# Kernel tuning notes

Measured on AMD Instinct MI355X. Metric: run time of the kernel, lower is better.

The kernel has to match this reference:

```python
import jax, jax.numpy as jnp
import numpy as np

CLIP_MIN = 0.0  # recurrent_clip_min resolved in build() when -1
CLIP_MAX = 1.0  # recurrent_clip_max default when timesteps unknown


def setup_inputs() -> dict:
    key = jax.random.key(0)
    k1, k2, k3 = jax.random.split(key, 3)
    B, T, D, U = 64, 512, 256, 512
    x = jax.random.normal(k1, (B, T, D), dtype=jnp.float32)
    h0 = jnp.zeros((B, U), dtype=jnp.float32)
    W = jax.random.normal(k2, (D, U), dtype=jnp.float32) * (1.0 / np.sqrt(D))
    u = jax.random.uniform(k3, (U,), dtype=jnp.float32)  # uniform in clip range
    b = jnp.zeros((U,), dtype=jnp.float32)
    return {"x": x, "h0": h0, "W": W, "u": u, "b": b}


def reference(x, h0, W, u, b):
    # IndRNN: h_t = relu(x_t @ W + h_{t-1} * u + b), u clipped to [0, 1]
    u_c = jnp.clip(u, CLIP_MIN, CLIP_MAX)
    # One-time input projection for all timesteps: [B,T,U]
    proj = jnp.einsum("btd,du->btu", x, W) + b
    proj_t = jnp.swapaxes(proj, 0, 1)  # [T,B,U] for scan over time

    def step(h, p_t):
        h_new = jax.nn.relu(p_t + h * u_c)
        return h_new, h_new

    _, hs = jax.lax.scan(step, h0, proj_t)  # hs: [T,B,U]
    return jnp.swapaxes(hs, 0, 1)  # [B,T,U]
```

## Files before the change

### kernel.cpp

```cpp
#include <hip/hip_runtime.h>


__device__ __forceinline__ unsigned short f2bf(float f) {
    unsigned int u = __float_as_uint(f);
    unsigned int r = (u + 0x7FFF + ((u >> 16) & 1)) >> 16;
    return (unsigned short)r;
}

typedef __bf16 bf16x8 __attribute__((ext_vector_type(8)));
typedef float f32x4 __attribute__((ext_vector_type(4)));

typedef const unsigned char __attribute__((address_space(1))) gc_t;
typedef unsigned char __attribute__((address_space(3))) lds_t;

__device__ __forceinline__ void gl_lds16(const void* g, void* l) {
    __builtin_amdgcn_global_load_lds((gc_t*)g, (lds_t*)l, 16, 0, 0);
}

__global__ __launch_bounds__(256) void conv_x(
    const float* __restrict__ x, unsigned short* __restrict__ xb, int n4)
{
    int i = blockIdx.x * blockDim.x + threadIdx.x;
    if (i >= n4) return;
    float4 v = *(const float4*)(x + (long)i * 4);
    ushort4 o;
    o.x = f2bf(v.x); o.y = f2bf(v.y); o.z = f2bf(v.z); o.w = f2bf(v.w);
    *(ushort4*)(xb + (long)i * 4) = o;
}

__global__ __launch_bounds__(256) void conv_wt(
    const float* __restrict__ W, unsigned short* __restrict__ Wt, int K, int N)
{
    int idx = blockIdx.x * blockDim.x + threadIdx.x;
    int kq = K >> 2;
    if (idx >= N * kq) return;
    int n = idx / kq;
    int k4 = (idx - n * kq) * 4;
    ushort4 o;
    o.x = f2bf(W[(long)(k4 + 0) * N + n]);
    o.y = f2bf(W[(long)(k4 + 1) * N + n]);
    o.z = f2bf(W[(long)(k4 + 2) * N + n]);
    o.w = f2bf(W[(long)(k4 + 3) * N + n]);
    *(ushort4*)(Wt + (long)n * K + k4) = o;
}

#define TC 64
#define GN 128

__global__ __launch_bounds__(256, 1) void indrnn_fused(
    const unsigned short* __restrict__ xb,
    const unsigned short* __restrict__ wt,
    const float* __restrict__ bias,
    const float* __restrict__ h0,
    const float* __restrict__ uvec,
    float* __restrict__ out,
    int B, int T, int U)
{
    __shared__ char Xs[TC * 512];
    __shared__ char Ps[GN * TC * 4];

    const int tid  = threadIdx.x;
    const int lane = tid & 63;
    const int w    = tid >> 6;
    const int m    = lane & 15;
    const int quad = lane >> 4;
    const int b    = blockIdx.x;
    const int n0   = blockIdx.y * GN;
    const int tq   = (w >> 1) * 32;
    const int cq   = (w & 1) * 64;

    bf16x8 bfr[4][8];
#pragma unroll
    for (int j = 0; j < 4; ++j)
#pragma unroll
        for (int kt = 0; kt < 8; ++kt)
            bfr[j][kt] = *(const bf16x8*)(
                wt + (long)(n0 + cq + j * 16 + m) * 256 + kt * 32 + quad * 8);

    float bb[4];
#pragma unroll
    for (int j = 0; j < 4; ++j) bb[j] = bias[n0 + cq + j * 16 + m];

    float uc = 0.0f, h = 0.0f;
    if (tid < GN) {
        uc = fminf(fmaxf(uvec[n0 + tid], 0.0f), 1.0f);
        h  = h0[(long)b * U + n0 + tid];
    }

    const unsigned short* xrow = xb + (long)b * T * 256;
    const int p  = lane & 31;
    const int hh = lane >> 5;

#pragma unroll
    for (int i = 0; i < 8; ++i) {
        int blk = i * 4 + w;
        int row = blk * 2 + hh;
        int gp  = p ^ (row & 15);
        gl_lds16(xrow + (long)row * 256 + gp * 8, &Xs[blk * 1024]);
    }
    asm volatile("s_waitcnt vmcnt(0)" ::: "memory");
    __builtin_amdgcn_sched_barrier(0);
    __syncthreads();

    const int nch = T / TC;
    for (int c = 0; c < nch; ++c) {
        f32x4 acc[2][4];
#pragma unroll
        for (int i = 0; i < 2; ++i)
#pragma unroll
            for (int j = 0; j < 4; ++j) acc[i][j] = (f32x4){0.f, 0.f, 0.f, 0.f};

#pragma unroll
        for (int kt = 0; kt < 8; ++kt) {
            const int off = (((kt * 4 + quad) ^ m) * 16);
            bf16x8 a0 = *(const bf16x8*)(Xs + (tq + m) * 512 + off);
            bf16x8 a1 = *(const bf16x8*)(Xs + (tq + 16 + m) * 512 + off);
#pragma unroll
            for (int j = 0; j < 4; ++j) {
                acc[0][j] = __builtin_amdgcn_mfma_f32_16x16x32_bf16(
                    a0, bfr[j][kt], acc[0][j], 0, 0, 0);
                acc[1][j] = __builtin_amdgcn_mfma_f32_16x16x32_bf16(
                    a1, bfr[j][kt], acc[1][j], 0, 0, 0);
            }
        }

#pragma unroll
        for (int i = 0; i < 2; ++i)
#pragma unroll
            for (int j = 0; j < 4; ++j) {
                f32x4 v = acc[i][j];
                f32x4 vb = {v[0] + bb[j], v[1] + bb[j], v[2] + bb[j], v[3] + bb[j]};
                int col = cq + j * 16 + m;
                int g   = (tq >> 2) + i * 4 + quad;
                *(f32x4*)(Ps + col * 256 + (((g ^ (col & 7)) << 4))) = vb;
            }
        __syncthreads();

        if (c + 1 < nch) {
            const unsigned short* gb = xrow + (long)(c + 1) * TC * 256;
#pragma unroll
            for (int i = 0; i < 8; ++i) {
                int blk = i * 4 + w;
                int row = blk * 2 + hh;
                int gp  = p ^ (row & 15);
                gl_lds16(gb + (long)row * 256 + gp * 8, &Xs[blk * 1024]);
            }
        }

        if (tid < GN) {
            f32x4 pv[16];
            const int ub = tid * 256;
            const int ux = (tid & 7) << 4;
#pragma unroll
            for (int gg = 0; gg < 16; ++gg)
                pv[gg] = *(const f32x4*)(Ps + ub + ((gg << 4) ^ ux));
            float* og = out + ((long)b * T + c * TC) * U + n0 + tid;
#pragma unroll
            for (int gg = 0; gg < 16; ++gg)
#pragma unroll
                for (int e = 0; e < 4; ++e) {
                    h = fmaxf(fmaf(h, uc, pv[gg][e]), 0.0f);
                    og[(long)(gg * 4 + e) * U] = h;
                }
        }

        asm volatile("s_waitcnt vmcnt(0)" ::: "memory");
        __builtin_amdgcn_sched_barrier(0);
        __syncthreads();
    }
}

#define BM 128
#define BN 128
#define BK 8

__global__ __launch_bounds__(256) void indrnn_gemm_bias(
    const float* __restrict__ A, const float* __restrict__ Bm,
    const float* __restrict__ bias, float* __restrict__ C,
    int M, int N, int K)
{
    __shared__ float As[BK][BM];
    __shared__ float Bs[BK][BN];
    const int tid = threadIdx.x;
    const int row0 = blockIdx.x * BM, col0 = blockIdx.y * BN;
    const int tx = tid & 15, ty = tid >> 4;
    float acc[8][8];
#pragma unroll
    for (int i = 0; i < 8; ++i)
#pragma unroll
        for (int j = 0; j < 8; ++j) acc[i][j] = 0.0f;
    const int am = tid >> 1, ak = (tid & 1) * 4;
    const int bk = tid >> 5, bn = (tid & 31) * 4;
    const float* Aptr = A + (long)(row0 + am) * K + ak;
    const float* Bptr = Bm + (long)bk * N + col0 + bn;
    for (int kt = 0; kt < K; kt += BK) {
        float4 av = *(const float4*)(Aptr + kt);
        float4 bv = *(const float4*)(Bptr + (long)kt * N);
        As[ak + 0][am] = av.x; As[ak + 1][am] = av.y;
        As[ak + 2][am] = av.z; As[ak + 3][am] = av.w;
        *(float4*)&Bs[bk][bn] = bv;
        __syncthreads();
#pragma unroll
        for (int k = 0; k < BK; ++k) {
            float4 a0 = *(const float4*)&As[k][ty * 4];
            float4 a1 = *(const float4*)&As[k][64 + ty * 4];
            float4 b0 = *(const float4*)&Bs[k][tx * 4];
            float4 b1 = *(const float4*)&Bs[k][64 + tx * 4];
            float a[8] = {a0.x, a0.y, a0.z, a0.w, a1.x, a1.y, a1.z, a1.w};
            float bb2[8] = {b0.x, b0.y, b0.z, b0.w, b1.x, b1.y, b1.z, b1.w};
#pragma unroll
            for (int i = 0; i < 8; ++i)
#pragma unroll
                for (int j = 0; j < 8; ++j)
                    acc[i][j] = fmaf(a[i], bb2[j], acc[i][j]);
        }
        __syncthreads();
    }
    float bb[8];
#pragma unroll
    for (int j = 0; j < 4; ++j) {
        bb[j] = bias[col0 + tx * 4 + j];
        bb[j + 4] = bias[col0 + 64 + tx * 4 + j];
    }
#pragma unroll
    for (int i = 0; i < 8; ++i) {
        const int r = (i < 4) ? (ty * 4 + i) : (64 + ty * 4 + (i - 4));
        float* crow = C + (long)(row0 + r) * N + col0;
        float4 v0 = {acc[i][0] + bb[0], acc[i][1] + bb[1], acc[i][2] + bb[2], acc[i][3] + bb[3]};
        float4 v1 = {acc[i][4] + bb[4], acc[i][5] + bb[5], acc[i][6] + bb[6], acc[i][7] + bb[7]};
        *(float4*)(crow + tx * 4) = v0;
        *(float4*)(crow + 64 + tx * 4) = v1;
    }
}

#define SCAN_UNROLL 32

__global__ __launch_bounds__(256) void indrnn_scan(
    float* __restrict__ out, const float* __restrict__ h0,
    const float* __restrict__ u, int B, int T, int U)
{
    const int idx = blockIdx.x * blockDim.x + threadIdx.x;
    if (idx >= B * U) return;
    const int b = idx / U;
    const int un = idx - b * U;
    const float uc = fminf(fmaxf(u[un], 0.0f), 1.0f);
    float h = h0[(long)b * U + un];
    float* p = out + (long)b * T * U + un;
    for (int t = 0; t < T; t += SCAN_UNROLL) {
        float pv[SCAN_UNROLL];
#pragma unroll
        for (int i = 0; i < SCAN_UNROLL; ++i)
            pv[i] = p[(long)(t + i) * U];
#pragma unroll
        for (int i = 0; i < SCAN_UNROLL; ++i) {
            h = fmaxf(fmaf(h, uc, pv[i]), 0.0f);
            pv[i] = h;
        }
#pragma unroll
        for (int i = 0; i < SCAN_UNROLL; ++i)
            p[(long)(t + i) * U] = pv[i];
    }
}

extern "C" void kernel_launch(void* const* d_in, const int* in_sizes, int n_in,
                              void* d_out, int out_size, void* d_ws, size_t ws_size,
                              hipStream_t stream) {
    const float* x  = (const float*)d_in[0];
    const float* h0 = (const float*)d_in[1];
    const float* W  = (const float*)d_in[2];
    const float* u  = (const float*)d_in[3];
    const float* b  = (const float*)d_in[4];
    float* out = (float*)d_out;

    const int U = in_sizes[3];
    const int B = in_sizes[1] / U;
    const int D = in_sizes[2] / U;
    const int T = in_sizes[0] / (B * D);
    const int M = B * T;

    const size_t xb_bytes = (size_t)M * D * sizeof(unsigned short);
    const size_t wt_bytes = (size_t)U * D * sizeof(unsigned short);
    const bool fused_ok = (D == 256) && (U % GN == 0) && (T % TC == 0) &&
                          (ws_size >= xb_bytes + wt_bytes);

    if (fused_ok) {
        unsigned short* xb = (unsigned short*)d_ws;
        unsigned short* wt = (unsigned short*)((char*)d_ws + xb_bytes);

        const int n4 = (M * D) / 4;
        conv_x<<<(n4 + 255) / 256, 256, 0, stream>>>(x, xb, n4);
        const int nwt = U * (D / 4);
        conv_wt<<<(nwt + 255) / 256, 256, 0, stream>>>(W, wt, D, U);

        dim3 g(B, U / GN);
        indrnn_fused<<<g, 256, 0, stream>>>(xb, wt, b, h0, u, out, B, T, U);
    } else {
        dim3 ggrid(M / BM, U / BN);
        indrnn_gemm_bias<<<ggrid, 256, 0, stream>>>(x, W, b, out, M, U, D);
        const int nthreads = B * U;
        indrnn_scan<<<(nthreads + 255) / 256, 256, 0, stream>>>(out, h0, u, B, T, U);
    }
}
```

Baseline: 118.7 us.

## Warp-specialize fused IndRNN into producer GEMM and consumer scan waves

Splits the fused kernel's four waves into two producer waves that do the bf16 MFMA projection and two consumer waves that run the sequential scan and write output. Double-buffered LDS tiles and shared-memory flag spin-waits replace the per-chunk __syncthreads, so the next chunk's GEMM can overlap the current chunk's scan. It also merges the two bf16 conversion kernels into one launch. Producer waves now hold all of the B fragments (bfr[8][8]), which raises register pressure. The volatile LDS polling depends on memory-ordering assumptions that could be fragile.

```diff
diff --git a/kernel.cpp b/kernel.cpp
--- a/kernel.cpp
+++ b/kernel.cpp
@@ -17,31 +17,31 @@
     __builtin_amdgcn_global_load_lds((gc_t*)g, (lds_t*)l, 16, 0, 0);
 }
 
-__global__ __launch_bounds__(256) void conv_x(
-    const float* __restrict__ x, unsigned short* __restrict__ xb, int n4)
+__global__ __launch_bounds__(256) void conv_xw(
+    const float* __restrict__ x, unsigned short* __restrict__ xb, int n4,
+    const float* __restrict__ W, unsigned short* __restrict__ Wt,
+    int K, int N, int xblocks)
 {
-    int i = blockIdx.x * blockDim.x + threadIdx.x;
-    if (i >= n4) return;
-    float4 v = *(const float4*)(x + (long)i * 4);
-    ushort4 o;
-    o.x = f2bf(v.x); o.y = f2bf(v.y); o.z = f2bf(v.z); o.w = f2bf(v.w);
-    *(ushort4*)(xb + (long)i * 4) = o;
-}
-
-__global__ __launch_bounds__(256) void conv_wt(
-    const float* __restrict__ W, unsigned short* __restrict__ Wt, int K, int N)
-{
-    int idx = blockIdx.x * blockDim.x + threadIdx.x;
-    int kq = K >> 2;
-    if (idx >= N * kq) return;
-    int n = idx / kq;
-    int k4 = (idx - n * kq) * 4;
-    ushort4 o;
-    o.x = f2bf(W[(long)(k4 + 0) * N + n]);
-    o.y = f2bf(W[(long)(k4 + 1) * N + n]);
-    o.z = f2bf(W[(long)(k4 + 2) * N + n]);
-    o.w = f2bf(W[(long)(k4 + 3) * N + n]);
-    *(ushort4*)(Wt + (long)n * K + k4) = o;
+    if ((int)blockIdx.x < xblocks) {
+        int i = blockIdx.x * 256 + threadIdx.x;
+        if (i >= n4) return;
+        float4 v = *(const float4*)(x + (long)i * 4);
+        ushort4 o;
+        o.x = f2bf(v.x); o.y = f2bf(v.y); o.z = f2bf(v.z); o.w = f2bf(v.w);
+        *(ushort4*)(xb + (long)i * 4) = o;
+    } else {
+        int idx = (blockIdx.x - xblocks) * 256 + threadIdx.x;
+        int kq = K >> 2;
+        if (idx >= N * kq) return;
+        int n = idx / kq;
+        int k4 = (idx - n * kq) * 4;
+        ushort4 o;
+        o.x = f2bf(W[(long)(k4 + 0) * N + n]);
+        o.y = f2bf(W[(long)(k4 + 1) * N + n]);
+        o.z = f2bf(W[(long)(k4 + 2) * N + n]);
+        o.w = f2bf(W[(long)(k4 + 3) * N + n]);
+        *(ushort4*)(Wt + (long)n * K + k4) = o;
+    }
 }
 
 #define TC 64
@@ -56,8 +56,9 @@
     float* __restrict__ out,
     int B, int T, int U)
 {
-    __shared__ char Xs[TC * 512];
-    __shared__ char Ps[GN * TC * 4];
+    __shared__ char Xs[2][TC * 512];
+    __shared__ char Ps[2][GN * TC * 4];
+    __shared__ int  flg[8];
 
     const int tid  = threadIdx.x;
     const int lane = tid & 63;
@@ -66,94 +67,112 @@
     const int quad = lane >> 4;
     const int b    = blockIdx.x;
     const int n0   = blockIdx.y * GN;
-    const int tq   = (w >> 1) * 32;
-    const int cq   = (w & 1) * 64;
-
-    bf16x8 bfr[4][8];
-#pragma unroll
-    for (int j = 0; j < 4; ++j)
-#pragma unroll
-        for (int kt = 0; kt < 8; ++kt)
-            bfr[j][kt] = *(const bf16x8*)(
-                wt + (long)(n0 + cq + j * 16 + m) * 256 + kt * 32 + quad * 8);
-
-    float bb[4];
-#pragma unroll
-    for (int j = 0; j < 4; ++j) bb[j] = bias[n0 + cq + j * 16 + m];
-
-    float uc = 0.0f, h = 0.0f;
-    if (tid < GN) {
-        uc = fminf(fmaxf(uvec[n0 + tid], 0.0f), 1.0f);
-        h  = h0[(long)b * U + n0 + tid];
-    }
-
-    const unsigned short* xrow = xb + (long)b * T * 256;
-    const int p  = lane & 31;
-    const int hh = lane >> 5;
-
-#pragma unroll
-    for (int i = 0; i < 8; ++i) {
-        int blk = i * 4 + w;
-        int row = blk * 2 + hh;
-        int gp  = p ^ (row & 15);
-        gl_lds16(xrow + (long)row * 256 + gp * 8, &Xs[blk * 1024]);
-    }
-    asm volatile("s_waitcnt vmcnt(0)" ::: "memory");
-    __builtin_amdgcn_sched_barrier(0);
+
+    if (tid < 8) flg[tid] = 0;
     __syncthreads();
 
+    volatile int* vf = (volatile int*)flg;
     const int nch = T / TC;
-    for (int c = 0; c < nch; ++c) {
-        f32x4 acc[2][4];
-#pragma unroll
-        for (int i = 0; i < 2; ++i)
-#pragma unroll
-            for (int j = 0; j < 4; ++j) acc[i][j] = (f32x4){0.f, 0.f, 0.f, 0.f};
-
-#pragma unroll
-        for (int kt = 0; kt < 8; ++kt) {
-            const int off = (((kt * 4 + quad) ^ m) * 16);
-            bf16x8 a0 = *(const bf16x8*)(Xs + (tq + m) * 512 + off);
-            bf16x8 a1 = *(const bf16x8*)(Xs + (tq + 16 + m) * 512 + off);
-#pragma unroll
-            for (int j = 0; j < 4; ++j) {
-                acc[0][j] = __builtin_amdgcn_mfma_f32_16x16x32_bf16(
-                    a0, bfr[j][kt], acc[0][j], 0, 0, 0);
-                acc[1][j] = __builtin_amdgcn_mfma_f32_16x16x32_bf16(
-                    a1, bfr[j][kt], acc[1][j], 0, 0, 0);
+
+    if (w >= 2) {
+        const int r0 = (w - 2) * 32;
+        const int p  = lane & 31;
+        const int hh = lane >> 5;
+        const unsigned short* xrow = xb + (long)b * T * 256;
+
+        bf16x8 bfr[8][8];
+#pragma unroll
+        for (int j = 0; j < 8; ++j)
+#pragma unroll
+            for (int kt = 0; kt < 8; ++kt)
+                bfr[j][kt] = *(const bf16x8*)(
+                    wt + (long)(n0 + j * 16 + m) * 256 + kt * 32 + quad * 8);
+
+        float bb[8];
+#pragma unroll
+        for (int j = 0; j < 8; ++j) bb[j] = bias[n0 + j * 16 + m];
+
+#pragma unroll
+        for (int l = 0; l < 16; ++l) {
+            int row = r0 + l * 2 + hh;
+            int gp  = p ^ (row & 15);
+            gl_lds16(xrow + (long)row * 256 + gp * 8,
+                     &Xs[0][r0 * 512 + l * 1024]);
+        }
+
+        for (int c = 0; c < nch; ++c) {
+            const int buf = c & 1, nb = buf ^ 1;
+
+            asm volatile("s_waitcnt vmcnt(0)" ::: "memory");
+            __builtin_amdgcn_sched_barrier(0);
+
+            if (c + 1 < nch) {
+                const unsigned short* gb = xrow + (long)(c + 1) * TC * 256;
+#pragma unroll
+                for (int l = 0; l < 16; ++l) {
+                    int row = r0 + l * 2 + hh;
+                    int gp  = p ^ (row & 15);
+                    gl_lds16(gb + (long)row * 256 + gp * 8,
+                             &Xs[nb][r0 * 512 + l * 1024]);
+                }
             }
-        }
-
-#pragma unroll
-        for (int i = 0; i < 2; ++i)
-#pragma unroll
-            for (int j = 0; j < 4; ++j) {
-                f32x4 v = acc[i][j];
-                f32x4 vb = {v[0] + bb[j], v[1] + bb[j], v[2] + bb[j], v[3] + bb[j]};
-                int col = cq + j * 16 + m;
-                int g   = (tq >> 2) + i * 4 + quad;
-                *(f32x4*)(Ps + col * 256 + (((g ^ (col & 7)) << 4))) = vb;
+
+            f32x4 acc[2][8];
+#pragma unroll
+            for (int i = 0; i < 2; ++i)
+#pragma unroll
+                for (int j = 0; j < 8; ++j) acc[i][j] = (f32x4){0.f, 0.f, 0.f, 0.f};
+
+#pragma unroll
+            for (int kt = 0; kt < 8; ++kt) {
+                const int off = (((kt * 4 + quad) ^ m) * 16);
+                bf16x8 a0 = *(const bf16x8*)(&Xs[buf][(r0 + m) * 512 + off]);
+                bf16x8 a1 = *(const bf16x8*)(&Xs[buf][(r0 + 16 + m) * 512 + off]);
+#pragma unroll
+                for (int j = 0; j < 8; ++j) {
+                    acc[0][j] = __builtin_amdgcn_mfma_f32_16x16x32_bf16(
+                        a0, bfr[j][kt], acc[0][j], 0, 0, 0);
+                    acc[1][j] = __builtin_amdgcn_mfma_f32_16x16x32_bf16(
+                        a1, bfr[j][kt], acc[1][j], 0, 0, 0);
+                }
             }
-        __syncthreads();
-
-        if (c + 1 < nch) {
-            const unsigned short* gb = xrow + (long)(c + 1) * TC * 256;
-#pragma unroll
-            for (int i = 0; i < 8; ++i) {
-                int blk = i * 4 + w;
-                int row = blk * 2 + hh;
-                int gp  = p ^ (row & 15);
-                gl_lds16(gb + (long)row * 256 + gp * 8, &Xs[blk * 1024]);
-            }
-        }
-
-        if (tid < GN) {
+
+            while (vf[4 + buf] < c - 1 || vf[6 + buf] < c - 1) {}
+            asm volatile("" ::: "memory");
+            __builtin_amdgcn_sched_barrier(0);
+
+#pragma unroll
+            for (int i = 0; i < 2; ++i)
+#pragma unroll
+                for (int j = 0; j < 8; ++j) {
+                    f32x4 v = acc[i][j];
+                    f32x4 vb = {v[0] + bb[j], v[1] + bb[j],
+                                v[2] + bb[j], v[3] + bb[j]};
+                    int col = j * 16 + m;
+                    int g   = (r0 >> 2) + i * 4 + quad;
+                    *(f32x4*)(&Ps[buf][col * 256 + (((g ^ (col & 7)) << 4))]) = vb;
+                }
+            asm volatile("s_waitcnt lgkmcnt(0)" ::: "memory");
+            if (lane == 0) vf[(w - 2) * 2 + buf] = c + 1;
+        }
+    } else {
+        const float uc = fminf(fmaxf(uvec[n0 + tid], 0.0f), 1.0f);
+        float h = h0[(long)b * U + n0 + tid];
+        const int ub = tid * 256;
+        const int ux = (tid & 7) << 4;
+
+        for (int c = 0; c < nch; ++c) {
+            const int buf = c & 1;
+
+            while (vf[0 + buf] < c + 1 || vf[2 + buf] < c + 1) {}
+            asm volatile("" ::: "memory");
+            __builtin_amdgcn_sched_barrier(0);
+
             f32x4 pv[16];
-            const int ub = tid * 256;
-            const int ux = (tid & 7) << 4;
 #pragma unroll
             for (int gg = 0; gg < 16; ++gg)
-                pv[gg] = *(const f32x4*)(Ps + ub + ((gg << 4) ^ ux));
+                pv[gg] = *(const f32x4*)(&Ps[buf][ub + ((gg << 4) ^ ux)]);
+
             float* og = out + ((long)b * T + c * TC) * U + n0 + tid;
 #pragma unroll
             for (int gg = 0; gg < 16; ++gg)
@@ -162,11 +181,10 @@
                     h = fmaxf(fmaf(h, uc, pv[gg][e]), 0.0f);
                     og[(long)(gg * 4 + e) * U] = h;
                 }
-        }
-
-        asm volatile("s_waitcnt vmcnt(0)" ::: "memory");
-        __builtin_amdgcn_sched_barrier(0);
-        __syncthreads();
+
+            asm volatile("s_waitcnt lgkmcnt(0)" ::: "memory");
+            if (lane == 0) vf[4 + w * 2 + buf] = c + 1;
+        }
     }
 }
 
@@ -288,9 +306,11 @@
         unsigned short* wt = (unsigned short*)((char*)d_ws + xb_bytes);
 
         const int n4 = (M * D) / 4;
-        conv_x<<<(n4 + 255) / 256, 256, 0, stream>>>(x, xb, n4);
         const int nwt = U * (D / 4);
-        conv_wt<<<(nwt + 255) / 256, 256, 0, stream>>>(W, wt, D, U);
+        const int xblocks = (n4 + 255) / 256;
+        const int wblocks = (nwt + 255) / 256;
+        conv_xw<<<xblocks + wblocks, 256, 0, stream>>>(
+            x, xb, n4, W, wt, D, U, xblocks);
 
         dim3 g(B, U / GN);
         indrnn_fused<<<g, 256, 0, stream>>>(xb, wt, b, h0, u, out, B, T, U);
```

Measured after the change: 121.5 us. +2.4%, slower.

## Fuse bf16 conversion of x and W into the fused IndRNN kernel

Applied to the files above, without the earlier changes.

Removes the separate conv_x and conv_wt pre-passes and the workspace round trip. The fused kernel now streams fp32 x rows straight into LDS with a wider swizzled layout and converts to bf16 in registers just before the MFMAs. W is gathered and converted per block at kernel start. The aim is to drop two kernel launches and the extra global write and read of a bf16 copy of x. In exchange, each block reads twice as many bytes of x, LDS use doubles, and every timestep chunk now does conversion work in the inner loop.

```diff
diff --git a/kernel.cpp b/kernel.cpp
--- a/kernel.cpp
+++ b/kernel.cpp
@@ -1,11 +1,5 @@
 #include <hip/hip_runtime.h>
 
-
-__device__ __forceinline__ unsigned short f2bf(float f) {
-    unsigned int u = __float_as_uint(f);
-    unsigned int r = (u + 0x7FFF + ((u >> 16) & 1)) >> 16;
-    return (unsigned short)r;
-}
 
 typedef __bf16 bf16x8 __attribute__((ext_vector_type(8)));
 typedef float f32x4 __attribute__((ext_vector_type(4)));
@@ -17,46 +11,28 @@
     __builtin_amdgcn_global_load_lds((gc_t*)g, (lds_t*)l, 16, 0, 0);
 }
 
-__global__ __launch_bounds__(256) void conv_x(
-    const float* __restrict__ x, unsigned short* __restrict__ xb, int n4)
-{
-    int i = blockIdx.x * blockDim.x + threadIdx.x;
-    if (i >= n4) return;
-    float4 v = *(const float4*)(x + (long)i * 4);
-    ushort4 o;
-    o.x = f2bf(v.x); o.y = f2bf(v.y); o.z = f2bf(v.z); o.w = f2bf(v.w);
-    *(ushort4*)(xb + (long)i * 4) = o;
-}
-
-__global__ __launch_bounds__(256) void conv_wt(
-    const float* __restrict__ W, unsigned short* __restrict__ Wt, int K, int N)
-{
-    int idx = blockIdx.x * blockDim.x + threadIdx.x;
-    int kq = K >> 2;
-    if (idx >= N * kq) return;
-    int n = idx / kq;
-    int k4 = (idx - n * kq) * 4;
-    ushort4 o;
-    o.x = f2bf(W[(long)(k4 + 0) * N + n]);
-    o.y = f2bf(W[(long)(k4 + 1) * N + n]);
-    o.z = f2bf(W[(long)(k4 + 2) * N + n]);
-    o.w = f2bf(W[(long)(k4 + 3) * N + n]);
-    *(ushort4*)(Wt + (long)n * K + k4) = o;
+__device__ __forceinline__ bf16x8 cvt8(f32x4 lo, f32x4 hi) {
+    bf16x8 r;
+    r[0] = (__bf16)lo[0]; r[1] = (__bf16)lo[1];
+    r[2] = (__bf16)lo[2]; r[3] = (__bf16)lo[3];
+    r[4] = (__bf16)hi[0]; r[5] = (__bf16)hi[1];
+    r[6] = (__bf16)hi[2]; r[7] = (__bf16)hi[3];
+    return r;
 }
 
 #define TC 64
 #define GN 128
 
 __global__ __launch_bounds__(256, 1) void indrnn_fused(
-    const unsigned short* __restrict__ xb,
-    const unsigned short* __restrict__ wt,
+    const float* __restrict__ x,
+    const float* __restrict__ W,
     const float* __restrict__ bias,
     const float* __restrict__ h0,
     const float* __restrict__ uvec,
     float* __restrict__ out,
     int B, int T, int U)
 {
-    __shared__ char Xs[TC * 512];
+    __shared__ char Xs[TC * 1024];
     __shared__ char Ps[GN * TC * 4];
 
     const int tid  = threadIdx.x;
@@ -69,13 +45,27 @@
     const int tq   = (w >> 1) * 32;
     const int cq   = (w & 1) * 64;
 
+    const float* xrow = x + (long)b * T * 256;
+
+#pragma unroll
+    for (int i = 0; i < 16; ++i) {
+        int row = i * 4 + w;
+        int sg  = lane ^ (row & 15);
+        gl_lds16(xrow + (long)row * 256 + sg * 4, &Xs[row * 1024]);
+    }
+
     bf16x8 bfr[4][8];
 #pragma unroll
     for (int j = 0; j < 4; ++j)
 #pragma unroll
-        for (int kt = 0; kt < 8; ++kt)
-            bfr[j][kt] = *(const bf16x8*)(
-                wt + (long)(n0 + cq + j * 16 + m) * 256 + kt * 32 + quad * 8);
+        for (int kt = 0; kt < 8; ++kt) {
+            const float* wp = W + (long)(kt * 32 + quad * 8) * U
+                                + (n0 + cq + j * 16 + m);
+            bf16x8 f;
+#pragma unroll
+            for (int e = 0; e < 8; ++e) f[e] = (__bf16)wp[(long)e * U];
+            bfr[j][kt] = f;
+        }
 
     float bb[4];
 #pragma unroll
@@ -87,17 +77,6 @@
         h  = h0[(long)b * U + n0 + tid];
     }
 
-    const unsigned short* xrow = xb + (long)b * T * 256;
-    const int p  = lane & 31;
-    const int hh = lane >> 5;
-
-#pragma unroll
-    for (int i = 0; i < 8; ++i) {
-        int blk = i * 4 + w;
-        int row = blk * 2 + hh;
-        int gp  = p ^ (row & 15);
-        gl_lds16(xrow + (long)row * 256 + gp * 8, &Xs[blk * 1024]);
-    }
     asm volatile("s_waitcnt vmcnt(0)" ::: "memory");
     __builtin_amdgcn_sched_barrier(0);
     __syncthreads();
@@ -112,9 +91,16 @@
 
 #pragma unroll
         for (int kt = 0; kt < 8; ++kt) {
-            const int off = (((kt * 4 + quad) ^ m) * 16);
-            bf16x8 a0 = *(const bf16x8*)(Xs + (tq + m) * 512 + off);
-            bf16x8 a1 = *(const bf16x8*)(Xs + (tq + 16 + m) * 512 + off);
+            const int g0 = ((kt * 8 + quad * 2 + 0) ^ m) << 4;
+            const int g1 = ((kt * 8 + quad * 2 + 1) ^ m) << 4;
+            const char* r0p = Xs + (tq + m) * 1024;
+            const char* r1p = Xs + (tq + 16 + m) * 1024;
+            f32x4 a0lo = *(const f32x4*)(r0p + g0);
+            f32x4 a0hi = *(const f32x4*)(r0p + g1);
+            f32x4 a1lo = *(const f32x4*)(r1p + g0);
+            f32x4 a1hi = *(const f32x4*)(r1p + g1);
+            bf16x8 a0 = cvt8(a0lo, a0hi);
+            bf16x8 a1 = cvt8(a1lo, a1hi);
 #pragma unroll
             for (int j = 0; j < 4; ++j) {
                 acc[0][j] = __builtin_amdgcn_mfma_f32_16x16x32_bf16(
@@ -137,13 +123,12 @@
         __syncthreads();
 
         if (c + 1 < nch) {
-            const unsigned short* gb = xrow + (long)(c + 1) * TC * 256;
-#pragma unroll
-            for (int i = 0; i < 8; ++i) {
-                int blk = i * 4 + w;
-                int row = blk * 2 + hh;
-                int gp  = p ^ (row & 15);
-                gl_lds16(gb + (long)row * 256 + gp * 8, &Xs[blk * 1024]);
+            const float* gb = xrow + (long)(c + 1) * TC * 256;
+#pragma unroll
+            for (int i = 0; i < 16; ++i) {
+                int row = i * 4 + w;
+                int sg  = lane ^ (row & 15);
+                gl_lds16(gb + (long)row * 256 + sg * 4, &Xs[row * 1024]);
             }
         }
 
@@ -278,22 +263,11 @@
     const int T = in_sizes[0] / (B * D);
     const int M = B * T;
 
-    const size_t xb_bytes = (size_t)M * D * sizeof(unsigned short);
-    const size_t wt_bytes = (size_t)U * D * sizeof(unsigned short);
-    const bool fused_ok = (D == 256) && (U % GN == 0) && (T % TC == 0) &&
-                          (ws_size >= xb_bytes + wt_bytes);
+    const bool fused_ok = (D == 256) && (U % GN == 0) && (T % TC == 0);
 
     if (fused_ok) {
-        unsigned short* xb = (unsigned short*)d_ws;
-        unsigned short* wt = (unsigned short*)((char*)d_ws + xb_bytes);
-
-        const int n4 = (M * D) / 4;
-        conv_x<<<(n4 + 255) / 256, 256, 0, stream>>>(x, xb, n4);
-        const int nwt = U * (D / 4);
-        conv_wt<<<(nwt + 255) / 256, 256, 0, stream>>>(W, wt, D, U);
-
         dim3 g(B, U / GN);
-        indrnn_fused<<<g, 256, 0, stream>>>(xb, wt, b, h0, u, out, B, T, U);
+        indrnn_fused<<<g, 256, 0, stream>>>(x, W, b, h0, u, out, B, T, U);
     } else {
         dim3 ggrid(M / BM, U / BN);
         indrnn_gemm_bias<<<ggrid, 256, 0, stream>>>(x, W, b, out, M, U, D);
```

Measured after the change: 116.4 us. No clear change (-1.9%).

## Double-buffer X chunks in LDS and fold W conversion into fused kernel

Applied to the files above, without the earlier changes.

Removes the separate conv_wt launch, so the fused kernel now reads fp32 W directly and converts it to bf16 in registers while the first X chunk is loading. The X staging buffer in LDS becomes double-buffered, and the next chunk's prefetch is issued before the MFMA work so it overlaps both the GEMM and the serial scan. The scan threads now wait with a partial vmcnt so their output stores are not drained every chunk. The risks are a doubled LDS footprint, strided scalar W loads at kernel start, and an fp32-to-bf16 cast whose rounding may differ from f2bf.

```diff
diff --git a/kernel.cpp b/kernel.cpp
--- a/kernel.cpp
+++ b/kernel.cpp
@@ -28,35 +28,19 @@
     *(ushort4*)(xb + (long)i * 4) = o;
 }
 
-__global__ __launch_bounds__(256) void conv_wt(
-    const float* __restrict__ W, unsigned short* __restrict__ Wt, int K, int N)
-{
-    int idx = blockIdx.x * blockDim.x + threadIdx.x;
-    int kq = K >> 2;
-    if (idx >= N * kq) return;
-    int n = idx / kq;
-    int k4 = (idx - n * kq) * 4;
-    ushort4 o;
-    o.x = f2bf(W[(long)(k4 + 0) * N + n]);
-    o.y = f2bf(W[(long)(k4 + 1) * N + n]);
-    o.z = f2bf(W[(long)(k4 + 2) * N + n]);
-    o.w = f2bf(W[(long)(k4 + 3) * N + n]);
-    *(ushort4*)(Wt + (long)n * K + k4) = o;
-}
-
 #define TC 64
 #define GN 128
 
 __global__ __launch_bounds__(256, 1) void indrnn_fused(
     const unsigned short* __restrict__ xb,
-    const unsigned short* __restrict__ wt,
+    const float* __restrict__ W,
     const float* __restrict__ bias,
     const float* __restrict__ h0,
     const float* __restrict__ uvec,
     float* __restrict__ out,
     int B, int T, int U)
 {
-    __shared__ char Xs[TC * 512];
+    __shared__ char Xs[2][TC * 512];
     __shared__ char Ps[GN * TC * 4];
 
     const int tid  = threadIdx.x;
@@ -69,13 +53,30 @@
     const int tq   = (w >> 1) * 32;
     const int cq   = (w & 1) * 64;
 
+    const unsigned short* xrow = xb + (long)b * T * 256;
+    const int p  = lane & 31;
+    const int hh = lane >> 5;
+
+#pragma unroll
+    for (int i = 0; i < 8; ++i) {
+        int blk = i * 4 + w;
+        int row = blk * 2 + hh;
+        int gp  = p ^ (row & 15);
+        gl_lds16(xrow + (long)row * 256 + gp * 8, &Xs[0][blk * 1024]);
+    }
+
     bf16x8 bfr[4][8];
 #pragma unroll
     for (int j = 0; j < 4; ++j)
 #pragma unroll
-        for (int kt = 0; kt < 8; ++kt)
-            bfr[j][kt] = *(const bf16x8*)(
-                wt + (long)(n0 + cq + j * 16 + m) * 256 + kt * 32 + quad * 8);
+        for (int kt = 0; kt < 8; ++kt) {
+            const float* wp = W + (long)(kt * 32 + quad * 8) * U
+                                + (n0 + cq + j * 16 + m);
+            bf16x8 f;
+#pragma unroll
+            for (int e = 0; e < 8; ++e) f[e] = (__bf16)wp[(long)e * U];
+            bfr[j][kt] = f;
+        }
 
     float bb[4];
 #pragma unroll
@@ -87,23 +88,25 @@
         h  = h0[(long)b * U + n0 + tid];
     }
 
-    const unsigned short* xrow = xb + (long)b * T * 256;
-    const int p  = lane & 31;
-    const int hh = lane >> 5;
-
-#pragma unroll
-    for (int i = 0; i < 8; ++i) {
-        int blk = i * 4 + w;
-        int row = blk * 2 + hh;
-        int gp  = p ^ (row & 15);
-        gl_lds16(xrow + (long)row * 256 + gp * 8, &Xs[blk * 1024]);
-    }
     asm volatile("s_waitcnt vmcnt(0)" ::: "memory");
     __builtin_amdgcn_sched_barrier(0);
     __syncthreads();
 
     const int nch = T / TC;
     for (int c = 0; c < nch; ++c) {
+        const int buf = c & 1;
+
+        if (c + 1 < nch) {
+            const unsigned short* gb = xrow + (long)(c + 1) * TC * 256;
+#pragma unroll
+            for (int i = 0; i < 8; ++i) {
+                int blk = i * 4 + w;
+                int row = blk * 2 + hh;
+                int gp  = p ^ (row & 15);
+                gl_lds16(gb + (long)row * 256 + gp * 8, &Xs[buf ^ 1][blk * 1024]);
+            }
+        }
+
         f32x4 acc[2][4];
 #pragma unroll
         for (int i = 0; i < 2; ++i)
@@ -113,8 +116,8 @@
 #pragma unroll
         for (int kt = 0; kt < 8; ++kt) {
             const int off = (((kt * 4 + quad) ^ m) * 16);
-            bf16x8 a0 = *(const bf16x8*)(Xs + (tq + m) * 512 + off);
-            bf16x8 a1 = *(const bf16x8*)(Xs + (tq + 16 + m) * 512 + off);
+            bf16x8 a0 = *(const bf16x8*)(&Xs[buf][(tq + m) * 512 + off]);
+            bf16x8 a1 = *(const bf16x8*)(&Xs[buf][(tq + 16 + m) * 512 + off]);
 #pragma unroll
             for (int j = 0; j < 4; ++j) {
                 acc[0][j] = __builtin_amdgcn_mfma_f32_16x16x32_bf16(
@@ -136,17 +139,6 @@
             }
         __syncthreads();
 
-        if (c + 1 < nch) {
-            const unsigned short* gb = xrow + (long)(c + 1) * TC * 256;
-#pragma unroll
-            for (int i = 0; i < 8; ++i) {
-                int blk = i * 4 + w;
-                int row = blk * 2 + hh;
-                int gp  = p ^ (row & 15);
-                gl_lds16(gb + (long)row * 256 + gp * 8, &Xs[blk * 1024]);
-            }
-        }
-
         if (tid < GN) {
             f32x4 pv[16];
             const int ub = tid * 256;
@@ -164,7 +156,11 @@
                 }
         }
 
-        asm volatile("s_waitcnt vmcnt(0)" ::: "memory");
+        if (tid < GN) {
+            asm volatile("s_waitcnt vmcnt(48)" ::: "memory");
+        } else {
+            asm volatile("s_waitcnt vmcnt(0)" ::: "memory");
+        }
         __builtin_amdgcn_sched_barrier(0);
         __syncthreads();
     }
@@ -279,21 +275,16 @@
     const int M = B * T;
 
     const size_t xb_bytes = (size_t)M * D * sizeof(unsigned short);
-    const size_t wt_bytes = (size_t)U * D * sizeof(unsigned short);
     const bool fused_ok = (D == 256) && (U % GN == 0) && (T % TC == 0) &&
-                          (ws_size >= xb_bytes + wt_bytes);
+                          (ws_size >= xb_bytes);
 
     if (fused_ok) {
         unsigned short* xb = (unsigned short*)d_ws;
-        unsigned short* wt = (unsigned short*)((char*)d_ws + xb_bytes);
-
         const int n4 = (M * D) / 4;
         conv_x<<<(n4 + 255) / 256, 256, 0, stream>>>(x, xb, n4);
-        const int nwt = U * (D / 4);
-        conv_wt<<<(nwt + 255) / 256, 256, 0, stream>>>(W, wt, D, U);
 
         dim3 g(B, U / GN);
-        indrnn_fused<<<g, 256, 0, stream>>>(xb, wt, b, h0, u, out, B, T, U);
+        indrnn_fused<<<g, 256, 0, stream>>>(xb, W, b, h0, u, out, B, T, U);
     } else {
         dim3 ggrid(M / BM, U / BN);
         indrnn_gemm_bias<<<ggrid, 256, 0, stream>>>(x, W, b, out, M, U, D);
```

Result: no change. 117.2 us (-1.3%).
